# Kernel tuning notes

Hardware: AMD Instinct MI355X
Metric: run time of the kernel (lower is better)

## Reference

```python
import jax, jax.numpy as jnp
import numpy as np

NUM_GT = 25      # num_gt_lesions (init kwarg); labels 1..25 all present in gt
NUM_PRED = 40    # number of predicted CC labels (labels 0..40 in pred)
SMOOTH = 1.0
VOL = (256, 256, 256)


def setup_inputs() -> dict:
    key = jax.random.key(0)
    k1, k2 = jax.random.split(key)
    # pred holds integer-valued connected-component labels stored as float
    # (the original applies sigmoid to it and compares values for identity).
    pred = jax.random.randint(k1, VOL, 0, NUM_PRED + 1).astype(jnp.float32)
    gt = jax.random.randint(k2, VOL, 0, NUM_GT + 1).astype(jnp.int32)
    return {"pred": pred, "gt": gt}


def _instance_dice(pred, gt):
    # Original: s = sigmoid(pred); all unique/isin/!=0 tests are on s.
    # sigmoid is injective => value equality on s == label equality on pred;
    # sigmoid(x) != 0 always  => every `!= 0` filter in the original is a no-op
    # (in particular pred label 0 participates, since sigmoid(0)=0.5).
    lbl = jax.lax.stop_gradient(jnp.round(pred)).astype(jnp.int32)  # pred CC ids
    g = gt.astype(jnp.int32)

    # Joint histogram counts[p, c] = #voxels with pred==p and gt==c.
    combined = (lbl * (NUM_GT + 1) + g).ravel()
    counts = jnp.zeros((NUM_PRED + 1) * (NUM_GT + 1), jnp.float32)
    counts = counts.at[combined].add(1.0).reshape(NUM_PRED + 1, NUM_GT + 1)

    gt_sizes = counts[:, 1:].sum(axis=0)            # [L] |gt == c| for c=1..L
    present = gt_sizes > 0
    num_gt = present.sum()                          # torch.unique(gt[gt!=0]).size(0)

    overlap = counts[:, 1:] > 0                     # [P+1, L] pred label p hits comp c
    pred_sizes = counts.sum(axis=1)                 # [P+1] |pred == p|
    union_size = (overlap * pred_sizes[:, None]).sum(axis=0)  # |pred_tmp| per comp
    # pred_tmp covers every voxel of the gt component => intersection = gt_sizes
    dice = 2.0 * gt_sizes / (union_size + gt_sizes + SMOOTH)
    lesion_dice = jnp.where(present, dice, 0.0).sum()

    tp_any = (overlap & present[None, :]).any(axis=1)  # pred labels collected in tp
    fp = ((pred_sizes > 0) & ~tp_any).sum()            # pred labels missing all gt comps
    return lesion_dice / (num_gt + fp)


def reference(pred, gt):
    return _instance_dice(pred, gt)
```

## Files before the change

kernel.cpp:

```cpp
#include <hip/hip_runtime.h>
#include <hip/hip_bf16.h>

#define NUM_GT 25
#define NUM_PRED 40
#define PAD 32

#define GT_W(b)  ((b) * PAD)
#define PR_W(p)  ((25 + (p)) * PAD)
#define OV_W(p)  ((65 + (p)) * PAD)
#define WS_WORDS (106 * PAD)

#define GRID  1024
#define BLOCK 256
#define TILE  2048

#if defined(__has_builtin)
#  if __has_builtin(__builtin_amdgcn_sad_u8)
#    define SAD(A, W, K) (A) = __builtin_amdgcn_sad_u8((W), (K), (A))
#  endif
#endif
#ifndef SAD
#  define SAD(A, W, K) asm("v_sad_u8 %0, %1, %2, %0" : "+v"(A) : "v"(W), "s"(K))
#endif

#define AS1 __attribute__((address_space(1)))
#define AS3 __attribute__((address_space(3)))

#if defined(__has_builtin) && __has_builtin(__builtin_amdgcn_global_load_lds)
#define GLOAD(SRC, DST) \
    __builtin_amdgcn_global_load_lds((const AS1 unsigned*)(SRC), \
                                     (AS3 unsigned*)(DST), 16, 0, 0)
#else
#define GLOAD(SRC, DST)  \
    (*(uint4*)((DST) + (threadIdx.x & 63) * 4) = *(const uint4*)(SRC))
#endif

__global__ __launch_bounds__(BLOCK) void hist_kernel(
    const float* __restrict__ pred, const int* __restrict__ gt,
    unsigned* __restrict__ ws, int n)
{
    __shared__ unsigned lgt[2][TILE];
    __shared__ unsigned lpr[2][TILE];
    __shared__ unsigned sovl[64];
    __shared__ unsigned shist[66];

    const int tid  = threadIdx.x;
    const int lane = tid & 63;
    const int wid  = tid >> 6;

    if (tid < 64) sovl[tid] = 0u;
    if (tid < 66) shist[tid] = 0u;

    unsigned acc[66];
    #pragma unroll
    for (int j = 0; j < 66; ++j) acc[j] = 0u;

    const unsigned* __restrict__ gu = (const unsigned*)gt;
    const unsigned* __restrict__ pu = (const unsigned*)pred;
    const int ntiles = n / TILE;
    const int nt = (ntiles > (int)blockIdx.x)
                 ? (ntiles - (int)blockIdx.x + GRID - 1) / GRID : 0;

    __syncthreads();

    #define STAGE(K)                                                          \
    do {                                                                      \
        const size_t base = ((size_t)blockIdx.x + (size_t)(K) * GRID) * TILE  \
                          + wid * 512;                                        \
        const unsigned* sg = gu + base + lane * 4;                            \
        unsigned* dg = &lgt[(K) & 1][0] + wid * 512;                          \
        GLOAD(sg, dg); GLOAD(sg + 256, dg + 256);                             \
        const unsigned* sp = pu + base + lane * 4;                            \
        unsigned* dp = &lpr[(K) & 1][0] + wid * 512;                          \
        GLOAD(sp, dp); GLOAD(sp + 256, dp + 256);                             \
    } while (0)

    if (nt > 0) STAGE(0);
    if (nt > 1) STAGE(1);

    for (int k = 0; k < nt; ++k) {
        if (k + 1 < nt) asm volatile("s_waitcnt vmcnt(4)" ::: "memory");
        else            asm volatile("s_waitcnt vmcnt(0)" ::: "memory");
        __builtin_amdgcn_sched_barrier(0);

        const uint4* g4 = (const uint4*)(&lgt[k & 1][0] + wid * 512);
        const uint4* p4 = (const uint4*)(&lpr[k & 1][0] + wid * 512);
        #pragma unroll
        for (int h = 0; h < 2; ++h) {
            uint4 gw = g4[h * 64 + lane];
            uint4 pw = p4[h * 64 + lane];
            unsigned b0 = (unsigned)__uint_as_float(pw.x);
            unsigned b1 = (unsigned)__uint_as_float(pw.y);
            unsigned b2 = (unsigned)__uint_as_float(pw.z);
            unsigned b3 = (unsigned)__uint_as_float(pw.w);

            atomicOr(&sovl[b0 & 63], 1u << (gw.x & 31));
            atomicOr(&sovl[b1 & 63], 1u << (gw.y & 31));
            atomicOr(&sovl[b2 & 63], 1u << (gw.z & 31));
            atomicOr(&sovl[b3 & 63], 1u << (gw.w & 31));

            unsigned G = gw.x | (gw.y << 8) | (gw.z << 16) | (gw.w << 24);
            unsigned P = b0 | (b1 << 8) | (b2 << 16) | (b3 << 24);
            #pragma unroll
            for (int b = 0; b < 25; ++b) {
                const unsigned K = (unsigned)(b * 0x01010101u);
                SAD(acc[b], G, K);
            }
            #pragma unroll
            for (int b = 0; b < 40; ++b) {
                const unsigned K = (unsigned)(b * 0x01010101u);
                SAD(acc[25 + b], P, K);
            }
        }

        if (k + 2 < nt) {
            asm volatile("s_waitcnt lgkmcnt(0)" ::: "memory");
            __builtin_amdgcn_sched_barrier(0);
            STAGE(k + 2);
        }
    }
    #undef STAGE

    if (blockIdx.x == 0 && tid == 0) {
        for (int v = ntiles * TILE; v < n; ++v) {
            int p = (int)pred[v];
            int g = gt[v];
            for (int b = 0; b < 25; ++b) atomicAdd(&ws[GT_W(b)], (unsigned)abs(g - b));
            for (int b = 0; b < 40; ++b) atomicAdd(&ws[PR_W(b)], (unsigned)abs(p - b));
            atomicOr(&ws[OV_W(min(max(p, 0), NUM_PRED))], 1u << (g & 31));
        }
    }

    __syncthreads();
    unsigned (*stash)[16][34] = (unsigned(*)[16][34])(&lgt[0][0]);
    #pragma unroll
    for (int jp = 0; jp < 33; ++jp) {
        unsigned v = acc[2 * jp] | (acc[2 * jp + 1] << 16);
        v += __shfl_down(v, 32, 64);
        v += __shfl_down(v, 16, 64);
        if (lane < 16) stash[wid][lane][jp] = v;
    }
    __syncthreads();

    for (int i = tid; i < 33 * 16; i += BLOCK) {
        int jp = i >> 4, sl = i & 15;
        unsigned a = stash[0][sl][jp] + stash[1][sl][jp]
                   + stash[2][sl][jp] + stash[3][sl][jp];
        unsigned lo = a & 0xFFFFu, hi = a >> 16;
        lo += __shfl_down(lo, 8, 16);  hi += __shfl_down(hi, 8, 16);
        lo += __shfl_down(lo, 4, 16);  hi += __shfl_down(hi, 4, 16);
        lo += __shfl_down(lo, 2, 16);  hi += __shfl_down(hi, 2, 16);
        lo += __shfl_down(lo, 1, 16);  hi += __shfl_down(hi, 1, 16);
        if (sl == 0) {
            if (lo) atomicAdd(&shist[2 * jp], lo);
            if (hi && 2 * jp + 1 < 65) atomicAdd(&shist[2 * jp + 1], hi);
        }
    }
    __syncthreads();

    for (int i = tid; i < 65; i += BLOCK) {
        unsigned s = shist[i];
        if (s) atomicAdd(&ws[i * PAD], s);
    }
    if (tid < 41) {
        unsigned v = sovl[tid];
        if (v) atomicOr(&ws[OV_W(tid)], v);
    }
}

__global__ __launch_bounds__(64) void finish_kernel(
    const unsigned* __restrict__ ws, float* __restrict__ out, int n)
{
    __shared__ long long gg[25], gp[40], psz[41];
    __shared__ unsigned ov[41];
    const int lane = threadIdx.x;
    if (lane < 25) gg[lane] = (long long)ws[GT_W(lane)];
    if (lane < 40) gp[lane] = (long long)ws[PR_W(lane)];
    if (lane < 41) ov[lane] = ws[OV_W(lane)];
    __syncthreads();

    const long long N = n, Sg = gg[0], Sp = gp[0];

    if (lane < 41) {
        int P = lane;
        long long f;
        if (P == 0)       f = (N - gp[0] + gp[1]) / 2;
        else if (P <= 38) f = (gp[P - 1] - 2 * gp[P] + gp[P + 1]) / 2;
        else if (P == 39) f = (gp[38] - 2 * gp[39] + (40 * N - Sp)) / 2;
        else              f = (gp[39] - 39 * N + Sp) / 2;
        psz[P] = f;
    }
    __syncthreads();

    double dice = 0.0;
    int present = 0;
    if (lane < 25) {
        int L = lane + 1;
        long long gs;
        if (L <= 23)      gs = (gg[L - 1] - 2 * gg[L] + gg[L + 1]) / 2;
        else if (L == 24) gs = (gg[23] - 2 * gg[24] + (25 * N - Sg)) / 2;
        else              gs = (gg[24] - 24 * N + Sg) / 2;
        if (gs > 0) {
            present = 1;
            double un = 0.0;
            const unsigned bit = 1u << L;
            for (int p = 0; p < 41; ++p)
                if (ov[p] & bit) un += (double)psz[p];
            dice = 2.0 * (double)gs / (un + (double)gs + 1.0);
        }
    }
    int fp = 0;
    if (lane < 41) {
        if (psz[lane] > 0 && (ov[lane] & 0x3FFFFFEu) == 0) fp = 1;
    }

    int num_gt = __popcll(__ballot(present != 0));
    int nfp    = __popcll(__ballot(fp != 0));
    #pragma unroll
    for (int o = 32; o >= 1; o >>= 1) dice += __shfl_xor(dice, o, 64);

    if (lane == 0) out[0] = (float)(dice / (double)(num_gt + nfp));
}

extern "C" void kernel_launch(void* const* d_in, const int* in_sizes, int n_in,
                              void* d_out, int out_size, void* d_ws, size_t ws_size,
                              hipStream_t stream) {
    const float* pred = (const float*)d_in[0];
    const int* gt = (const int*)d_in[1];
    float* out = (float*)d_out;
    unsigned* ws = (unsigned*)d_ws;
    const int n = in_sizes[0];

    hipMemsetAsync(ws, 0, WS_WORDS * sizeof(unsigned), stream);

    hist_kernel<<<GRID, BLOCK, 0, stream>>>(pred, gt, ws, n);
    finish_kernel<<<1, 64, 0, stream>>>(ws, out, n);
}
```

Measured before the change: 45.39 us.

## Restructure LDS double-buffer to load registers first, then prefetch the next tile

Changes the software pipeline from two tiles in flight to one. Each iteration now reads the current tile from LDS into registers up front, issues the async global-to-LDS prefetch of the next tile into the other buffer, and then runs the SAD/atomic histogram work on the registers. The explicit vmcnt/lgkmcnt waits are removed, which relies on the compiler to add waits before reading LDS filled by the async DMA. If it does not, a race is possible. Prefetch depth also drops, so there is less load latency hidden behind compute.

```diff
diff --git a/kernel.cpp b/kernel.cpp
--- a/kernel.cpp
+++ b/kernel.cpp
@@ -31,7 +31,7 @@
     __builtin_amdgcn_global_load_lds((const AS1 unsigned*)(SRC), \
                                      (AS3 unsigned*)(DST), 16, 0, 0)
 #else
-#define GLOAD(SRC, DST)  \
+#define GLOAD(SRC, DST) \
     (*(uint4*)((DST) + (threadIdx.x & 63) * 4) = *(const uint4*)(SRC))
 #endif
 
@@ -76,30 +76,27 @@
     } while (0)
 
     if (nt > 0) STAGE(0);
-    if (nt > 1) STAGE(1);
 
     for (int k = 0; k < nt; ++k) {
-        if (k + 1 < nt) asm volatile("s_waitcnt vmcnt(4)" ::: "memory");
-        else            asm volatile("s_waitcnt vmcnt(0)" ::: "memory");
-        __builtin_amdgcn_sched_barrier(0);
-
         const uint4* g4 = (const uint4*)(&lgt[k & 1][0] + wid * 512);
         const uint4* p4 = (const uint4*)(&lpr[k & 1][0] + wid * 512);
-        #pragma unroll
-        for (int h = 0; h < 2; ++h) {
-            uint4 gw = g4[h * 64 + lane];
-            uint4 pw = p4[h * 64 + lane];
-            unsigned b0 = (unsigned)__uint_as_float(pw.x);
-            unsigned b1 = (unsigned)__uint_as_float(pw.y);
-            unsigned b2 = (unsigned)__uint_as_float(pw.z);
-            unsigned b3 = (unsigned)__uint_as_float(pw.w);
-
-            atomicOr(&sovl[b0 & 63], 1u << (gw.x & 31));
-            atomicOr(&sovl[b1 & 63], 1u << (gw.y & 31));
-            atomicOr(&sovl[b2 & 63], 1u << (gw.z & 31));
-            atomicOr(&sovl[b3 & 63], 1u << (gw.w & 31));
-
-            unsigned G = gw.x | (gw.y << 8) | (gw.z << 16) | (gw.w << 24);
+        uint4 gw0 = g4[lane],      pw0 = p4[lane];
+        uint4 gw1 = g4[64 + lane], pw1 = p4[64 + lane];
+        __builtin_amdgcn_sched_barrier(0);
+
+        if (k + 1 < nt) STAGE(k + 1);
+        __builtin_amdgcn_sched_barrier(0);
+
+        {
+            unsigned b0 = (unsigned)__uint_as_float(pw0.x);
+            unsigned b1 = (unsigned)__uint_as_float(pw0.y);
+            unsigned b2 = (unsigned)__uint_as_float(pw0.z);
+            unsigned b3 = (unsigned)__uint_as_float(pw0.w);
+            atomicOr(&sovl[b0 & 63], 1u << (gw0.x & 31));
+            atomicOr(&sovl[b1 & 63], 1u << (gw0.y & 31));
+            atomicOr(&sovl[b2 & 63], 1u << (gw0.z & 31));
+            atomicOr(&sovl[b3 & 63], 1u << (gw0.w & 31));
+            unsigned G = gw0.x | (gw0.y << 8) | (gw0.z << 16) | (gw0.w << 24);
             unsigned P = b0 | (b1 << 8) | (b2 << 16) | (b3 << 24);
             #pragma unroll
             for (int b = 0; b < 25; ++b) {
@@ -112,11 +109,27 @@
                 SAD(acc[25 + b], P, K);
             }
         }
-
-        if (k + 2 < nt) {
-            asm volatile("s_waitcnt lgkmcnt(0)" ::: "memory");
-            __builtin_amdgcn_sched_barrier(0);
-            STAGE(k + 2);
+        {
+            unsigned b0 = (unsigned)__uint_as_float(pw1.x);
+            unsigned b1 = (unsigned)__uint_as_float(pw1.y);
+            unsigned b2 = (unsigned)__uint_as_float(pw1.z);
+            unsigned b3 = (unsigned)__uint_as_float(pw1.w);
+            atomicOr(&sovl[b0 & 63], 1u << (gw1.x & 31));
+            atomicOr(&sovl[b1 & 63], 1u << (gw1.y & 31));
+            atomicOr(&sovl[b2 & 63], 1u << (gw1.z & 31));
+            atomicOr(&sovl[b3 & 63], 1u << (gw1.w & 31));
+            unsigned G = gw1.x | (gw1.y << 8) | (gw1.z << 16) | (gw1.w << 24);
+            unsigned P = b0 | (b1 << 8) | (b2 << 16) | (b3 << 24);
+            #pragma unroll
+            for (int b = 0; b < 25; ++b) {
+                const unsigned K = (unsigned)(b * 0x01010101u);
+                SAD(acc[b], G, K);
+            }
+            #pragma unroll
+            for (int b = 0; b < 40; ++b) {
+                const unsigned K = (unsigned)(b * 0x01010101u);
+                SAD(acc[25 + b], P, K);
+            }
         }
     }
     #undef STAGE
```

Result: no change. 45.34 us (-0.1%).
